# Kernel optimization log

Hardware: AMD Instinct MI355X
Metric: run time of the kernel (lower is better)

## Reference

```python
import jax, jax.numpy as jnp
import numpy as np

N_NODES = 50000


def _gcn_norm(edge_index):
    # symmetric GCN normalization 1/sqrt(deg_src*deg_dst), computed from edge list
    src, dst = edge_index[0], edge_index[1]
    ones = jnp.ones(src.shape[0], dtype=jnp.float32)
    deg = jax.ops.segment_sum(ones, dst, num_segments=N_NODES)
    deg = jnp.maximum(deg, 1.0)
    inv_sqrt = jax.lax.rsqrt(deg)
    return inv_sqrt[src] * inv_sqrt[dst]  # [E]


def _graph_conv(x, src, dst, norm, W, b):
    # gather messages from source nodes, normalize, scatter-add to destinations
    msgs = x[src] * norm[:, None]                       # [E, F]
    agg = jax.ops.segment_sum(msgs, dst, num_segments=N_NODES)  # [N, F]
    return agg @ W + b


def setup_inputs() -> dict:
    key = jax.random.key(0)
    ks = jax.random.split(key, 8)
    F, H, C, E = 128, 256, 40, 600000
    x = jax.random.normal(ks[0], (N_NODES, F), dtype=jnp.float32)
    edge_index = jax.random.randint(ks[1], (2, E), 0, N_NODES, dtype=jnp.int32)
    W1 = jax.random.normal(ks[2], (F, H), dtype=jnp.float32) * (1.0 / np.sqrt(F))
    b1 = jnp.zeros((H,), dtype=jnp.float32)
    W2 = jax.random.normal(ks[3], (H, H), dtype=jnp.float32) * (1.0 / np.sqrt(H))
    b2 = jnp.zeros((H,), dtype=jnp.float32)
    Wd = jax.random.normal(ks[4], (H, C), dtype=jnp.float32) * (1.0 / np.sqrt(H))
    bd = jnp.zeros((C,), dtype=jnp.float32)
    return {"x": x, "edge_index": edge_index, "W1": W1, "b1": b1,
            "W2": W2, "b2": b2, "Wd": Wd, "bd": bd}


def reference(x, edge_index, W1, b1, W2, b2, Wd, bd):
    src, dst = edge_index[0], edge_index[1]
    norm = _gcn_norm(edge_index)
    h = jax.nn.relu(_graph_conv(x, src, dst, norm, W1, b1))
    h = jax.nn.relu(_graph_conv(h, src, dst, norm, W2, b2))
    return jax.nn.softmax(h @ Wd + bd, axis=-1)
```

## Files before the change

kernel.cpp:

```cpp
#include <hip/hip_runtime.h>
#include <hip/hip_bf16.h>
#include <math.h>

#define N_NODES 50000

typedef short short8 __attribute__((ext_vector_type(8)));
typedef float f32x4 __attribute__((ext_vector_type(4)));

static __device__ __forceinline__ void split2(float x, unsigned short& hi, unsigned short& lo) {
    unsigned u = __builtin_bit_cast(unsigned, x);
    unsigned r = u + 0x7FFF + ((u >> 16) & 1);
    hi = (unsigned short)(r >> 16);
    float hf = __builtin_bit_cast(float, (unsigned)hi << 16);
    float res = x - hf;
    unsigned v = __builtin_bit_cast(unsigned, res);
    unsigned r2 = v + 0x7FFF + ((v >> 16) & 1);
    lo = (unsigned short)(r2 >> 16);
}


__global__ void deg_kernel(const int* __restrict__ dst, int* __restrict__ deg, int E) {
    int e = blockIdx.x * blockDim.x + threadIdx.x;
    if (e < E) atomicAdd(&deg[dst[e]], 1);
}


__global__ void scan_p1(const int* __restrict__ deg, int* __restrict__ bsum, int n) {
    int t = threadIdx.x;
    int base = blockIdx.x * 1024 + t * 4;
    int4 v = make_int4(0, 0, 0, 0);
    if (base + 3 < n) v = *(const int4*)(deg + base);
    else {
        if (base + 0 < n) v.x = deg[base + 0];
        if (base + 1 < n) v.y = deg[base + 1];
        if (base + 2 < n) v.z = deg[base + 2];
    }
    int s = v.x + v.y + v.z + v.w;
    #pragma unroll
    for (int off = 32; off > 0; off >>= 1) s += __shfl_xor(s, off);
    __shared__ int wpart[4];
    if ((t & 63) == 0) wpart[t >> 6] = s;
    __syncthreads();
    if (t == 0) bsum[blockIdx.x] = wpart[0] + wpart[1] + wpart[2] + wpart[3];
}

__global__ void scan_p2(int* __restrict__ bsum, int nb, int* __restrict__ rowptr, int n) {
    int t = threadIdx.x;
    int v = (t < nb) ? bsum[t] : 0;
    int sc = v;
    #pragma unroll
    for (int off = 1; off < 64; off <<= 1) {
        int u = __shfl_up(sc, off);
        if (t >= off) sc += u;
    }
    if (t < nb) bsum[t] = sc - v;
    if (t == 63) rowptr[n] = sc;
}

__global__ void scan_p3(const int* __restrict__ deg, const int* __restrict__ bsum,
                        int* __restrict__ rowptr, int* __restrict__ cursor,
                        float* __restrict__ inv, int n) {
    int t = threadIdx.x;
    int base = blockIdx.x * 1024 + t * 4;
    int4 v = make_int4(0, 0, 0, 0);
    if (base + 3 < n) v = *(const int4*)(deg + base);
    else {
        if (base + 0 < n) v.x = deg[base + 0];
        if (base + 1 < n) v.y = deg[base + 1];
        if (base + 2 < n) v.z = deg[base + 2];
    }
    int s = v.x + v.y + v.z + v.w;
    int lane = t & 63;
    int sc = s;
    #pragma unroll
    for (int off = 1; off < 64; off <<= 1) {
        int u = __shfl_up(sc, off);
        if (lane >= off) sc += u;
    }
    __shared__ int wpart[4], woff[4];
    if (lane == 63) wpart[t >> 6] = sc;
    __syncthreads();
    if (t == 0) { int a = 0; for (int i = 0; i < 4; ++i) { woff[i] = a; a += wpart[i]; } }
    __syncthreads();
    int run = bsum[blockIdx.x] + woff[t >> 6] + (sc - s);
    if (base + 0 < n) { rowptr[base + 0] = run; cursor[base + 0] = run; run += v.x; inv[base + 0] = rsqrtf(fmaxf((float)v.x, 1.0f)); }
    if (base + 1 < n) { rowptr[base + 1] = run; cursor[base + 1] = run; run += v.y; inv[base + 1] = rsqrtf(fmaxf((float)v.y, 1.0f)); }
    if (base + 2 < n) { rowptr[base + 2] = run; cursor[base + 2] = run; run += v.z; inv[base + 2] = rsqrtf(fmaxf((float)v.z, 1.0f)); }
    if (base + 3 < n) { rowptr[base + 3] = run; cursor[base + 3] = run; run += v.w; inv[base + 3] = rsqrtf(fmaxf((float)v.w, 1.0f)); }
}


__global__ void fill_kernel(const int* __restrict__ src, const int* __restrict__ dst,
                            const float* __restrict__ inv, int* __restrict__ cursor,
                            int2* __restrict__ edges, int E) {
    int e = blockIdx.x * blockDim.x + threadIdx.x;
    if (e >= E) return;
    int s = src[e];
    int d = dst[e];
    int pos = atomicAdd(&cursor[d], 1);
    float nv = inv[s] * inv[d];
    edges[pos] = make_int2(s, __builtin_bit_cast(int, nv));
}


__global__ void gather_agg_pass(const float* __restrict__ x, int coff, int ss,
                                const int* __restrict__ rowptr, const int2* __restrict__ edges,
                                unsigned short* __restrict__ agg_hi,
                                unsigned short* __restrict__ agg_lo, int as) {
    int node = blockIdx.x * 4 + (threadIdx.x >> 6);
    if (node >= N_NODES) return;
    int lane = threadIdx.x & 63;
    int beg = rowptr[node];
    int end = rowptr[node + 1];
    const float* xb = x + coff + (size_t)lane * 2;

    float2 acc = {0.0f, 0.0f};
    int p = beg;
    for (; p + 4 <= end; p += 4) {
        int2 e0 = edges[p], e1 = edges[p + 1], e2 = edges[p + 2], e3 = edges[p + 3];
        float n0 = __builtin_bit_cast(float, e0.y);
        float n1 = __builtin_bit_cast(float, e1.y);
        float n2 = __builtin_bit_cast(float, e2.y);
        float n3 = __builtin_bit_cast(float, e3.y);
        float2 v0 = *(const float2*)(xb + (size_t)e0.x * ss);
        float2 v1 = *(const float2*)(xb + (size_t)e1.x * ss);
        float2 v2 = *(const float2*)(xb + (size_t)e2.x * ss);
        float2 v3 = *(const float2*)(xb + (size_t)e3.x * ss);
        acc.x = fmaf(v0.x, n0, acc.x); acc.y = fmaf(v0.y, n0, acc.y);
        acc.x = fmaf(v1.x, n1, acc.x); acc.y = fmaf(v1.y, n1, acc.y);
        acc.x = fmaf(v2.x, n2, acc.x); acc.y = fmaf(v2.y, n2, acc.y);
        acc.x = fmaf(v3.x, n3, acc.x); acc.y = fmaf(v3.y, n3, acc.y);
    }
    for (; p < end; ++p) {
        int2 e0 = edges[p];
        float n0 = __builtin_bit_cast(float, e0.y);
        float2 v0 = *(const float2*)(xb + (size_t)e0.x * ss);
        acc.x = fmaf(v0.x, n0, acc.x);
        acc.y = fmaf(v0.y, n0, acc.y);
    }

    unsigned short h0, l0, h1, l1;
    split2(acc.x, h0, l0);
    split2(acc.y, h1, l1);
    unsigned hp = (unsigned)h0 | ((unsigned)h1 << 16);
    unsigned lp = (unsigned)l0 | ((unsigned)l1 << 16);
    size_t o = (size_t)node * as + coff + (size_t)lane * 2;
    *(unsigned*)(agg_hi + o) = hp;
    *(unsigned*)(agg_lo + o) = lp;
}


__global__ void split_w_all(const float* __restrict__ W1, const float* __restrict__ W2,
                            unsigned short* __restrict__ w1hi, unsigned short* __restrict__ w1lo,
                            unsigned short* __restrict__ w2hi, unsigned short* __restrict__ w2lo) {
    int i = blockIdx.x * 256 + threadIdx.x;
    if (i < 128 * 256) {
        int k = i >> 8;
        int n = i & 255;
        unsigned short h, l;
        split2(W1[i], h, l);
        w1hi[(size_t)n * 128 + k] = h;
        w1lo[(size_t)n * 128 + k] = l;
    } else {
        int j = i - 128 * 256;
        int k = j >> 8;
        int n = j & 255;
        unsigned short h, l;
        split2(W2[j], h, l);
        w2hi[(size_t)n * 256 + k] = h;
        w2lo[(size_t)n * 256 + k] = l;
    }
}


template<int K, bool RELU>
__global__ __launch_bounds__(256, 2) void gemm_mfma_kernel(
    const unsigned short* __restrict__ Ahi, const unsigned short* __restrict__ Alo,
    const unsigned short* __restrict__ Bhi, const unsigned short* __restrict__ Blo,
    const float* __restrict__ bias, float* __restrict__ out, int M)
{
    constexpr int ROWS = 128;
    __shared__ unsigned short AsH[2][ROWS][40];
    __shared__ unsigned short AsL[2][ROWS][40];

    int tid = threadIdx.x;
    int lane = tid & 63;
    int wave = tid >> 6;
    int row0 = blockIdx.x * ROWS;
    int col0 = wave * 64;
    int lr = lane & 15;
    int lhi = lane >> 4;
    int koff0 = lhi * 8;

    const unsigned short* Asrc = (tid < 128) ? Ahi : Alo;
    int s = tid & 127;
    int srow0 = s >> 2;
    int skg = (s & 3) << 3;

    f32x4 acc[4][8];
    #pragma unroll
    for (int i = 0; i < 4; ++i)
        #pragma unroll
        for (int j = 0; j < 8; ++j) acc[i][j] = (f32x4){0.f, 0.f, 0.f, 0.f};

    short8 rr[4];
    #pragma unroll
    for (int j = 0; j < 4; ++j)
        rr[j] = *(const short8*)(Asrc + (size_t)(row0 + j * 32 + srow0) * K + skg);
    #pragma unroll
    for (int j = 0; j < 4; ++j) {
        if (tid < 128) *(short8*)&AsH[0][j * 32 + srow0][skg] = rr[j];
        else           *(short8*)&AsL[0][j * 32 + srow0][skg] = rr[j];
    }
    __syncthreads();

    constexpr int NT = K / 32;
    #pragma unroll 1
    for (int t = 0; t < NT; ++t) {
        int cur = t & 1;
        int ko = t * 32 + koff0;

        short8 bh[4], bl[4];
        #pragma unroll
        for (int cf = 0; cf < 4; ++cf) {
            size_t boff = (size_t)(col0 + cf * 16 + lr) * K + ko;
            bh[cf] = *(const short8*)(Bhi + boff);
            bl[cf] = *(const short8*)(Blo + boff);
        }

        if (t + 1 < NT) {
            int kk = (t + 1) * 32;
            #pragma unroll
            for (int j = 0; j < 4; ++j)
                rr[j] = *(const short8*)(Asrc + (size_t)(row0 + j * 32 + srow0) * K + kk + skg);
        }

        #pragma unroll
        for (int half = 0; half < 2; ++half) {
            short8 ah[4], al[4];
            #pragma unroll
            for (int rf = 0; rf < 4; ++rf) {
                int row = (half * 4 + rf) * 16 + lr;
                ah[rf] = *(const short8*)&AsH[cur][row][koff0];
                al[rf] = *(const short8*)&AsL[cur][row][koff0];
            }
            #pragma unroll
            for (int cf = 0; cf < 4; ++cf)
                #pragma unroll
                for (int rf = 0; rf < 4; ++rf) {
                    int rfx = half * 4 + rf;
                    acc[cf][rfx] = __builtin_amdgcn_mfma_f32_16x16x32_bf16(bh[cf], ah[rf], acc[cf][rfx], 0, 0, 0);
                    acc[cf][rfx] = __builtin_amdgcn_mfma_f32_16x16x32_bf16(bl[cf], ah[rf], acc[cf][rfx], 0, 0, 0);
                    acc[cf][rfx] = __builtin_amdgcn_mfma_f32_16x16x32_bf16(bh[cf], al[rf], acc[cf][rfx], 0, 0, 0);
                }
        }

        if (t + 1 < NT) {
            #pragma unroll
            for (int j = 0; j < 4; ++j) {
                if (tid < 128) *(short8*)&AsH[cur ^ 1][j * 32 + srow0][skg] = rr[j];
                else           *(short8*)&AsL[cur ^ 1][j * 32 + srow0][skg] = rr[j];
            }
        }
        __syncthreads();
    }

    #pragma unroll
    for (int cf = 0; cf < 4; ++cf) {
        int c = col0 + cf * 16 + lhi * 4;
        float4 bv = *(const float4*)(bias + c);
        #pragma unroll
        for (int rfx = 0; rfx < 8; ++rfx) {
            int r = row0 + rfx * 16 + lr;
            if (r < M) {
                float4 v;
                v.x = acc[cf][rfx][0] + bv.x;
                v.y = acc[cf][rfx][1] + bv.y;
                v.z = acc[cf][rfx][2] + bv.z;
                v.w = acc[cf][rfx][3] + bv.w;
                if (RELU) {
                    v.x = fmaxf(v.x, 0.f); v.y = fmaxf(v.y, 0.f);
                    v.z = fmaxf(v.z, 0.f); v.w = fmaxf(v.w, 0.f);
                }
                *(float4*)(out + (size_t)r * 256 + c) = v;
            }
        }
    }
}


__global__ __launch_bounds__(256) void dense_softmax_kernel(const float* __restrict__ h,
                                                            const float* __restrict__ Wd,
                                                            const float* __restrict__ bd,
                                                            float* __restrict__ out, int M) {
    __shared__ float hs[32][260];
    __shared__ float wt[40][260];
    int tid = threadIdx.x;
    int row0 = blockIdx.x * 32;

    for (int i = tid; i < 40 * 256; i += 256) {
        int k = i / 40;
        int c = i - k * 40;
        wt[c][k] = Wd[i];
    }
    #pragma unroll
    for (int i = 0; i < 8; ++i) {
        int f = tid + i * 256;
        int r = f >> 6;
        int k4 = (f & 63) << 2;
        float4 v = make_float4(0.f, 0.f, 0.f, 0.f);
        if (row0 + r < M) v = *(const float4*)(h + (size_t)(row0 + r) * 256 + k4);
        *(float4*)&hs[r][k4] = v;
    }
    __syncthreads();

    int r  = tid >> 3;
    int cg = tid & 7;
    int c0 = cg * 5;

    float acc[5] = {0.f, 0.f, 0.f, 0.f, 0.f};
    #pragma unroll 4
    for (int k4 = 0; k4 < 64; ++k4) {
        float4 hv = *(float4*)&hs[r][k4 * 4];
        #pragma unroll
        for (int j = 0; j < 5; ++j) {
            float4 wv = *(float4*)&wt[c0 + j][k4 * 4];
            acc[j] = fmaf(hv.x, wv.x, acc[j]);
            acc[j] = fmaf(hv.y, wv.y, acc[j]);
            acc[j] = fmaf(hv.z, wv.z, acc[j]);
            acc[j] = fmaf(hv.w, wv.w, acc[j]);
        }
    }
    #pragma unroll
    for (int j = 0; j < 5; ++j) acc[j] += bd[c0 + j];

    float m = acc[0];
    #pragma unroll
    for (int j = 1; j < 5; ++j) m = fmaxf(m, acc[j]);
    #pragma unroll
    for (int off = 1; off < 8; off <<= 1) m = fmaxf(m, __shfl_xor(m, off));

    float e[5], s = 0.f;
    #pragma unroll
    for (int j = 0; j < 5; ++j) { e[j] = expf(acc[j] - m); s += e[j]; }
    #pragma unroll
    for (int off = 1; off < 8; off <<= 1) s += __shfl_xor(s, off);

    int row = row0 + r;
    if (row < M) {
        float inv_s = 1.0f / s;
        float* orow = out + (size_t)row * 40 + c0;
        #pragma unroll
        for (int j = 0; j < 5; ++j) orow[j] = e[j] * inv_s;
    }
}


extern "C" void kernel_launch(void* const* d_in, const int* in_sizes, int n_in,
                              void* d_out, int out_size, void* d_ws, size_t ws_size,
                              hipStream_t stream) {
    const float* x  = (const float*)d_in[0];
    const int*   ei = (const int*)d_in[1];
    const float* W1 = (const float*)d_in[2];
    const float* b1 = (const float*)d_in[3];
    const float* W2 = (const float*)d_in[4];
    const float* b2 = (const float*)d_in[5];
    const float* Wd = (const float*)d_in[6];
    const float* bd = (const float*)d_in[7];
    float* out = (float*)d_out;

    const int N = N_NODES;
    const int E = in_sizes[1] / 2;
    const int* src = ei;
    const int* dst = ei + E;

    const int MP = 50048;

    char* ws = (char*)d_ws;
    size_t off = 0;
    auto alloc = [&](size_t bytes) { char* p = ws + off; off += (bytes + 1023) & ~(size_t)1023; return p; };
    int*   deg    = (int*)alloc((size_t)N * 4);
    float* inv    = (float*)alloc((size_t)N * 4);
    int*   rowptr = (int*)alloc((size_t)(N + 1) * 4);
    int*   cursor = (int*)alloc((size_t)N * 4);
    int*   bsum   = (int*)alloc((size_t)64 * 4);
    int2*  edges  = (int2*)alloc((size_t)E * 8);
    float* h1     = (float*)alloc((size_t)N * 256 * 4);
    unsigned short* aggU = (unsigned short*)alloc((size_t)MP * 256 * 2 * 2);
    unsigned short* w1hi = (unsigned short*)alloc((size_t)128 * 256 * 2);
    unsigned short* w1lo = (unsigned short*)alloc((size_t)128 * 256 * 2);
    unsigned short* w2hi = (unsigned short*)alloc((size_t)256 * 256 * 2);
    unsigned short* w2lo = (unsigned short*)alloc((size_t)256 * 256 * 2);

    unsigned short* agg1_hi = aggU;
    unsigned short* agg1_lo = aggU + (size_t)MP * 128;
    unsigned short* agg2_hi = aggU;
    unsigned short* agg2_lo = aggU + (size_t)MP * 256;
    float* h2 = h1;

    hipMemsetAsync(deg, 0, (size_t)N * 4, stream);

    const int nb = (N + 1023) / 1024;

    deg_kernel<<<(E + 255) / 256, 256, 0, stream>>>(dst, deg, E);
    scan_p1<<<nb, 256, 0, stream>>>(deg, bsum, N);
    scan_p2<<<1, 64, 0, stream>>>(bsum, nb, rowptr, N);
    scan_p3<<<nb, 256, 0, stream>>>(deg, bsum, rowptr, cursor, inv, N);
    fill_kernel<<<(E + 255) / 256, 256, 0, stream>>>(src, dst, inv, cursor, edges, E);

    split_w_all<<<(128 * 256 + 256 * 256) / 256, 256, 0, stream>>>(W1, W2, w1hi, w1lo, w2hi, w2lo);

    const int gblocks = (N + 3) / 4;

    gather_agg_pass<<<gblocks, 256, 0, stream>>>(x, 0, 128, rowptr, edges, agg1_hi, agg1_lo, 128);
    gemm_mfma_kernel<128, true><<<MP / 128, 256, 0, stream>>>(agg1_hi, agg1_lo, w1hi, w1lo, b1, h1, N);

    gather_agg_pass<<<gblocks, 256, 0, stream>>>(h1, 0,   256, rowptr, edges, agg2_hi, agg2_lo, 256);
    gather_agg_pass<<<gblocks, 256, 0, stream>>>(h1, 128, 256, rowptr, edges, agg2_hi, agg2_lo, 256);
    gemm_mfma_kernel<256, true><<<MP / 128, 256, 0, stream>>>(agg2_hi, agg2_lo, w2hi, w2lo, b2, h2, N);

    dense_softmax_kernel<<<(N + 31) / 32, 256, 0, stream>>>(h2, Wd, bd, out, N);
}
```

Before: 306.9 us.

## Run final dense+softmax layer on MFMA with split-bf16 layer-2 output

The second GEMM now writes its ReLU output directly as hi/lo bf16 pairs, and the final 256x40 projection plus softmax is moved from an FP32 LDS-based kernel onto bf16x3 MFMA instructions. Wd is split and padded to 48 columns in the weight-prep kernel. This removes the scalar FMA work and the FP32 h2 store and reload, in exchange for an emulated-precision product and extra split work in the GEMM epilogue. The h1 buffer is enlarged to MP rows so that it can hold both split halves.

```diff
diff --git a/kernel.cpp b/kernel.cpp
--- a/kernel.cpp
+++ b/kernel.cpp
@@ -151,8 +151,10 @@
 
 
 __global__ void split_w_all(const float* __restrict__ W1, const float* __restrict__ W2,
+                            const float* __restrict__ Wd,
                             unsigned short* __restrict__ w1hi, unsigned short* __restrict__ w1lo,
-                            unsigned short* __restrict__ w2hi, unsigned short* __restrict__ w2lo) {
+                            unsigned short* __restrict__ w2hi, unsigned short* __restrict__ w2lo,
+                            unsigned short* __restrict__ wdhi, unsigned short* __restrict__ wdlo) {
     int i = blockIdx.x * 256 + threadIdx.x;
     if (i < 128 * 256) {
         int k = i >> 8;
@@ -161,7 +163,7 @@
         split2(W1[i], h, l);
         w1hi[(size_t)n * 128 + k] = h;
         w1lo[(size_t)n * 128 + k] = l;
-    } else {
+    } else if (i < 128 * 256 + 256 * 256) {
         int j = i - 128 * 256;
         int k = j >> 8;
         int n = j & 255;
@@ -169,15 +171,25 @@
         split2(W2[j], h, l);
         w2hi[(size_t)n * 256 + k] = h;
         w2lo[(size_t)n * 256 + k] = l;
-    }
-}
-
-
-template<int K, bool RELU>
+    } else {
+        int j = i - 128 * 256 - 256 * 256;
+        int c = j >> 8;
+        int k = j & 255;
+        float val = (c < 40) ? Wd[(size_t)k * 40 + c] : 0.0f;
+        unsigned short h, l;
+        split2(val, h, l);
+        wdhi[(size_t)c * 256 + k] = h;
+        wdlo[(size_t)c * 256 + k] = l;
+    }
+}
+
+
+template<int K, bool SPLIT_OUT>
 __global__ __launch_bounds__(256, 2) void gemm_mfma_kernel(
     const unsigned short* __restrict__ Ahi, const unsigned short* __restrict__ Alo,
     const unsigned short* __restrict__ Bhi, const unsigned short* __restrict__ Blo,
-    const float* __restrict__ bias, float* __restrict__ out, int M)
+    const float* __restrict__ bias, float* __restrict__ out,
+    unsigned short* __restrict__ outHi, unsigned short* __restrict__ outLo, int M)
 {
     constexpr int ROWS = 128;
     __shared__ unsigned short AsH[2][ROWS][40];
@@ -273,85 +285,110 @@
         for (int rfx = 0; rfx < 8; ++rfx) {
             int r = row0 + rfx * 16 + lr;
             if (r < M) {
-                float4 v;
-                v.x = acc[cf][rfx][0] + bv.x;
-                v.y = acc[cf][rfx][1] + bv.y;
-                v.z = acc[cf][rfx][2] + bv.z;
-                v.w = acc[cf][rfx][3] + bv.w;
-                if (RELU) {
-                    v.x = fmaxf(v.x, 0.f); v.y = fmaxf(v.y, 0.f);
-                    v.z = fmaxf(v.z, 0.f); v.w = fmaxf(v.w, 0.f);
+                float v0 = fmaxf(acc[cf][rfx][0] + bv.x, 0.f);
+                float v1 = fmaxf(acc[cf][rfx][1] + bv.y, 0.f);
+                float v2 = fmaxf(acc[cf][rfx][2] + bv.z, 0.f);
+                float v3 = fmaxf(acc[cf][rfx][3] + bv.w, 0.f);
+                if (!SPLIT_OUT) {
+                    float4 v = make_float4(v0, v1, v2, v3);
+                    *(float4*)(out + (size_t)r * 256 + c) = v;
+                } else {
+                    ushort4 hv, lv;
+                    split2(v0, hv.x, lv.x);
+                    split2(v1, hv.y, lv.y);
+                    split2(v2, hv.z, lv.z);
+                    split2(v3, hv.w, lv.w);
+                    *(ushort4*)(outHi + (size_t)r * 256 + c) = hv;
+                    *(ushort4*)(outLo + (size_t)r * 256 + c) = lv;
                 }
-                *(float4*)(out + (size_t)r * 256 + c) = v;
             }
         }
     }
 }
 
 
-__global__ __launch_bounds__(256) void dense_softmax_kernel(const float* __restrict__ h,
-                                                            const float* __restrict__ Wd,
-                                                            const float* __restrict__ bd,
-                                                            float* __restrict__ out, int M) {
-    __shared__ float hs[32][260];
-    __shared__ float wt[40][260];
+__global__ __launch_bounds__(256) void dense_mfma_kernel(
+    const unsigned short* __restrict__ Hhi, const unsigned short* __restrict__ Hlo,
+    const unsigned short* __restrict__ Dhi, const unsigned short* __restrict__ Dlo,
+    const float* __restrict__ bd, float* __restrict__ out, int M)
+{
     int tid = threadIdx.x;
-    int row0 = blockIdx.x * 32;
-
-    for (int i = tid; i < 40 * 256; i += 256) {
-        int k = i / 40;
-        int c = i - k * 40;
-        wt[c][k] = Wd[i];
-    }
-    #pragma unroll
-    for (int i = 0; i < 8; ++i) {
-        int f = tid + i * 256;
-        int r = f >> 6;
-        int k4 = (f & 63) << 2;
-        float4 v = make_float4(0.f, 0.f, 0.f, 0.f);
-        if (row0 + r < M) v = *(const float4*)(h + (size_t)(row0 + r) * 256 + k4);
-        *(float4*)&hs[r][k4] = v;
-    }
-    __syncthreads();
-
-    int r  = tid >> 3;
-    int cg = tid & 7;
-    int c0 = cg * 5;
-
-    float acc[5] = {0.f, 0.f, 0.f, 0.f, 0.f};
-    #pragma unroll 4
-    for (int k4 = 0; k4 < 64; ++k4) {
-        float4 hv = *(float4*)&hs[r][k4 * 4];
+    int lane = tid & 63;
+    int wave = tid >> 6;
+    int row0 = blockIdx.x * 64 + wave * 16;
+    int lr = lane & 15;
+    int lhi = lane >> 4;
+    int koff0 = lhi * 8;
+
+    f32x4 acc[3];
+    #pragma unroll
+    for (int i = 0; i < 3; ++i) acc[i] = (f32x4){0.f, 0.f, 0.f, 0.f};
+
+    size_t abase = (size_t)(row0 + lr) * 256 + koff0;
+    short8 ah = *(const short8*)(Hhi + abase);
+    short8 al = *(const short8*)(Hlo + abase);
+
+    #pragma unroll
+    for (int t = 0; t < 8; ++t) {
+        short8 ah2, al2;
+        if (t + 1 < 8) {
+            ah2 = *(const short8*)(Hhi + abase + (t + 1) * 32);
+            al2 = *(const short8*)(Hlo + abase + (t + 1) * 32);
+        }
+        int ko = t * 32 + koff0;
         #pragma unroll
-        for (int j = 0; j < 5; ++j) {
-            float4 wv = *(float4*)&wt[c0 + j][k4 * 4];
-            acc[j] = fmaf(hv.x, wv.x, acc[j]);
-            acc[j] = fmaf(hv.y, wv.y, acc[j]);
-            acc[j] = fmaf(hv.z, wv.z, acc[j]);
-            acc[j] = fmaf(hv.w, wv.w, acc[j]);
-        }
-    }
-    #pragma unroll
-    for (int j = 0; j < 5; ++j) acc[j] += bd[c0 + j];
-
-    float m = acc[0];
-    #pragma unroll
-    for (int j = 1; j < 5; ++j) m = fmaxf(m, acc[j]);
-    #pragma unroll
-    for (int off = 1; off < 8; off <<= 1) m = fmaxf(m, __shfl_xor(m, off));
-
-    float e[5], s = 0.f;
-    #pragma unroll
-    for (int j = 0; j < 5; ++j) { e[j] = expf(acc[j] - m); s += e[j]; }
-    #pragma unroll
-    for (int off = 1; off < 8; off <<= 1) s += __shfl_xor(s, off);
-
-    int row = row0 + r;
-    if (row < M) {
-        float inv_s = 1.0f / s;
-        float* orow = out + (size_t)row * 40 + c0;
-        #pragma unroll
-        for (int j = 0; j < 5; ++j) orow[j] = e[j] * inv_s;
+        for (int cf = 0; cf < 3; ++cf) {
+            size_t boff = (size_t)(cf * 16 + lr) * 256 + ko;
+            short8 bh = *(const short8*)(Dhi + boff);
+            short8 bl = *(const short8*)(Dlo + boff);
+            acc[cf] = __builtin_amdgcn_mfma_f32_16x16x32_bf16(bh, ah, acc[cf], 0, 0, 0);
+            acc[cf] = __builtin_amdgcn_mfma_f32_16x16x32_bf16(bl, ah, acc[cf], 0, 0, 0);
+            acc[cf] = __builtin_amdgcn_mfma_f32_16x16x32_bf16(bh, al, acc[cf], 0, 0, 0);
+        }
+        if (t + 1 < 8) { ah = ah2; al = al2; }
+    }
+
+    bool v2 = (lhi < 2);
+    float4 b0 = *(const float4*)(bd + lhi * 4);
+    float4 b1 = *(const float4*)(bd + 16 + lhi * 4);
+    float4 b2 = v2 ? *(const float4*)(bd + 32 + lhi * 4) : make_float4(0.f, 0.f, 0.f, 0.f);
+
+    float l0[4], l1[4], l2[4];
+    const float* pb0 = (const float*)&b0;
+    const float* pb1 = (const float*)&b1;
+    const float* pb2 = (const float*)&b2;
+    #pragma unroll
+    for (int j = 0; j < 4; ++j) {
+        l0[j] = acc[0][j] + pb0[j];
+        l1[j] = acc[1][j] + pb1[j];
+        l2[j] = v2 ? (acc[2][j] + pb2[j]) : -INFINITY;
+    }
+
+    float m = l0[0];
+    #pragma unroll
+    for (int j = 0; j < 4; ++j) { m = fmaxf(m, l0[j]); m = fmaxf(m, l1[j]); m = fmaxf(m, l2[j]); }
+    m = fmaxf(m, __shfl_xor(m, 16));
+    m = fmaxf(m, __shfl_xor(m, 32));
+
+    float e0[4], e1[4], e2[4];
+    float ssum = 0.f;
+    #pragma unroll
+    for (int j = 0; j < 4; ++j) {
+        e0[j] = expf(l0[j] - m); ssum += e0[j];
+        e1[j] = expf(l1[j] - m); ssum += e1[j];
+        e2[j] = v2 ? expf(l2[j] - m) : 0.f; ssum += e2[j];
+    }
+    ssum += __shfl_xor(ssum, 16);
+    ssum += __shfl_xor(ssum, 32);
+
+    int r = row0 + lr;
+    if (r < M) {
+        float is = 1.0f / ssum;
+        float* orow = out + (size_t)r * 40;
+        *(float4*)(orow + lhi * 4)      = make_float4(e0[0] * is, e0[1] * is, e0[2] * is, e0[3] * is);
+        *(float4*)(orow + 16 + lhi * 4) = make_float4(e1[0] * is, e1[1] * is, e1[2] * is, e1[3] * is);
+        if (v2)
+            *(float4*)(orow + 32 + lhi * 4) = make_float4(e2[0] * is, e2[1] * is, e2[2] * is, e2[3] * is);
     }
 }
 
@@ -385,18 +422,21 @@
     int*   cursor = (int*)alloc((size_t)N * 4);
     int*   bsum   = (int*)alloc((size_t)64 * 4);
     int2*  edges  = (int2*)alloc((size_t)E * 8);
-    float* h1     = (float*)alloc((size_t)N * 256 * 4);
+    float* h1     = (float*)alloc((size_t)MP * 256 * 4);
     unsigned short* aggU = (unsigned short*)alloc((size_t)MP * 256 * 2 * 2);
     unsigned short* w1hi = (unsigned short*)alloc((size_t)128 * 256 * 2);
     unsigned short* w1lo = (unsigned short*)alloc((size_t)128 * 256 * 2);
     unsigned short* w2hi = (unsigned short*)alloc((size_t)256 * 256 * 2);
     unsigned short* w2lo = (unsigned short*)alloc((size_t)256 * 256 * 2);
+    unsigned short* wdhi = (unsigned short*)alloc((size_t)48 * 256 * 2);
+    unsigned short* wdlo = (unsigned short*)alloc((size_t)48 * 256 * 2);
 
     unsigned short* agg1_hi = aggU;
     unsigned short* agg1_lo = aggU + (size_t)MP * 128;
     unsigned short* agg2_hi = aggU;
     unsigned short* agg2_lo = aggU + (size_t)MP * 256;
-    float* h2 = h1;
+    unsigned short* h2hi = (unsigned short*)h1;
+    unsigned short* h2lo = h2hi + (size_t)MP * 256;
 
     hipMemsetAsync(deg, 0, (size_t)N * 4, stream);
 
@@ -408,16 +448,19 @@
     scan_p3<<<nb, 256, 0, stream>>>(deg, bsum, rowptr, cursor, inv, N);
     fill_kernel<<<(E + 255) / 256, 256, 0, stream>>>(src, dst, inv, cursor, edges, E);
 
-    split_w_all<<<(128 * 256 + 256 * 256) / 256, 256, 0, stream>>>(W1, W2, w1hi, w1lo, w2hi, w2lo);
+    split_w_all<<<(128 * 256 + 256 * 256 + 48 * 256) / 256, 256, 0, stream>>>(
+        W1, W2, Wd, w1hi, w1lo, w2hi, w2lo, wdhi, wdlo);
 
     const int gblocks = (N + 3) / 4;
 
     gather_agg_pass<<<gblocks, 256, 0, stream>>>(x, 0, 128, rowptr, edges, agg1_hi, agg1_lo, 128);
-    gemm_mfma_kernel<128, true><<<MP / 128, 256, 0, stream>>>(agg1_hi, agg1_lo, w1hi, w1lo, b1, h1, N);
+    gemm_mfma_kernel<128, false><<<MP / 128, 256, 0, stream>>>(
+        agg1_hi, agg1_lo, w1hi, w1lo, b1, h1, nullptr, nullptr, N);
 
     gather_agg_pass<<<gblocks, 256, 0, stream>>>(h1, 0,   256, rowptr, edges, agg2_hi, agg2_lo, 256);
     gather_agg_pass<<<gblocks, 256, 0, stream>>>(h1, 128, 256, rowptr, edges, agg2_hi, agg2_lo, 256);
-    gemm_mfma_kernel<256, true><<<MP / 128, 256, 0, stream>>>(agg2_hi, agg2_lo, w2hi, w2lo, b2, h2, N);
-
-    dense_softmax_kernel<<<(N + 31) / 32, 256, 0, stream>>>(h2, Wd, bd, out, N);
-}
+    gemm_mfma_kernel<256, true><<<MP / 128, 256, 0, stream>>>(
+        agg2_hi, agg2_lo, w2hi, w2lo, b2, nullptr, h2hi, h2lo, N);
+
+    dense_mfma_kernel<<<MP / 64, 256, 0, stream>>>(h2hi, h2lo, wdhi, wdlo, bd, out, N);
+}
```

Result: no change. 308.1 us (+0.4%).
